# Optimization experiments

Measured on AMD Instinct MI355X. Metric: run time of the kernel, lower is better.

## Reference

```python
import jax, jax.numpy as jnp
import numpy as np


def setup_inputs() -> dict:
    key = jax.random.key(0)
    k1, k2, k3, k4 = jax.random.split(key, 4)
    batch, d_in, d_out, K, M = 4096, 1024, 1024, 16, 512
    x = jax.random.normal(k1, (batch, d_in), dtype=jnp.float32)
    A = jax.random.normal(k2, (K, d_in, M), dtype=jnp.float32) * (1.0 / np.sqrt(d_in))
    B = jax.random.normal(k3, (K, M, d_out), dtype=jnp.float32) * (1.0 / np.sqrt(M))
    bias = jnp.zeros((d_out,), dtype=jnp.float32)
    topk_mask = jax.random.randint(k4, (batch, K), 0, 2) > 0
    return {"x": x, "topk_mask": topk_mask, "A": A, "B": B, "bias": bias}


def reference(x, topk_mask, A, B, bias):
    # pre_inner_acts: [batch, k, m]
    pre = jnp.einsum('bi,kim->bkm', x, A)
    maskf = topk_mask.astype(pre.dtype)[:, :, None]  # [batch, k, 1]
    pre = pre * maskf
    # inner_acts: [batch, k, out]
    inner_acts = jnp.einsum('bkm,kmh->bkh', pre, B)
    inner_acts = inner_acts * maskf
    out = jnp.sum(inner_acts, axis=1) + bias  # [batch, out]
    return out, inner_acts
```

## Files before the change

kernel.cpp:

```cpp
#include <hip/hip_runtime.h>

typedef __attribute__((ext_vector_type(8))) short bf16x8;
typedef __attribute__((ext_vector_type(4))) float f32x4;

__device__ __forceinline__ unsigned short f2bf(float f) {
  union { float f; unsigned u; } v; v.f = f;
  unsigned r = v.u + 0x7fffu + ((v.u >> 16) & 1u);
  return (unsigned short)(r >> 16);
}

__global__ __launch_bounds__(256)
void prep_kernel(const float* __restrict__ x, unsigned short* __restrict__ x_bf,
                 const float* __restrict__ A, unsigned short* __restrict__ A_t,
                 const float* __restrict__ B, unsigned short* __restrict__ B_t,
                 const int* __restrict__ mask, int* __restrict__ rows,
                 int* __restrict__ counts) {
  __shared__ float tbuf[32][33];
  __shared__ int cnt, mcnt;
  const int bid = blockIdx.x;
  const int t = threadIdx.x;

  if (bid < 4096) {
    int i = bid * 256 + t;
    float4 v = ((const float4*)x)[i];
    ushort4 o; o.x = f2bf(v.x); o.y = f2bf(v.y); o.z = f2bf(v.z); o.w = f2bf(v.w);
    ((ushort4*)x_bf)[i] = o;
    return;
  }
  if (bid < 20480) {
    const float* in; unsigned short* out; int R, C, cx, ry, z;
    if (bid < 12288) {
      int local = (bid - 4096) & 511; z = (bid - 4096) >> 9;
      R = 1024; C = 512; cx = local & 15; ry = local >> 4;
      in = A; out = A_t;
    } else {
      int local = (bid - 12288) & 511; z = (bid - 12288) >> 9;
      R = 512; C = 1024; cx = local & 31; ry = local >> 5;
      in = B; out = B_t;
    }
    size_t eo = (size_t)z * R * C;
    const float* src = in + eo;
    unsigned short* dst = out + eo;
    int c0 = cx * 32, r0 = ry * 32;
    int tx = t & 31, ty = t >> 5;
#pragma unroll
    for (int i = 0; i < 32; i += 8)
      tbuf[ty + i][tx] = src[(size_t)(r0 + ty + i) * C + (c0 + tx)];
    __syncthreads();
#pragma unroll
    for (int i = 0; i < 32; i += 8)
      dst[(size_t)(c0 + ty + i) * R + (r0 + tx)] = f2bf(tbuf[tx][ty + i]);
    return;
  }
  {
    int z = bid - 20480;
    if (t == 0) { cnt = 0; mcnt = 0; }
    __syncthreads();
    int* rz = rows + (size_t)z * 4096;
    for (int i = t; i < 4096; i += 256) {
      bool m = mask[(size_t)i * 16 + z] != 0;
      unsigned long long bal = __ballot(m);
      int lane = t & 63;
      int pa = __popcll(bal & ((1ull << lane) - 1ull));
      int ta = __popcll(bal);
      int base_a, base_m;
      if (lane == 0) { base_a = atomicAdd(&cnt, ta); base_m = atomicAdd(&mcnt, 64 - ta); }
      base_a = __shfl(base_a, 0);
      base_m = __shfl(base_m, 0);
      int pm = lane - pa;
      if (m) rz[base_a + pa] = i;
      else   rz[4095 - (base_m + pm)] = i;
    }
    __syncthreads();
    if (t == 0) counts[z] = cnt;
  }
}

__device__ __forceinline__ void stage_tile(const unsigned short* __restrict__ src,
                                           size_t row_stride, int row0, int k0,
                                           unsigned short* lds) {
  int t = threadIdx.x;
  int lane = t & 63;
  int w = t >> 6;
#pragma unroll
  for (int i = 0; i < 4; ++i) {
    int chunk = w * 4 + i;
    int row = chunk * 8 + (lane >> 3);
    int glog = (lane & 7) ^ (row & 7);
    const unsigned short* g = src + (size_t)(row0 + row) * row_stride + (size_t)(k0 + glog * 8);
    __builtin_amdgcn_global_load_lds((const __attribute__((address_space(1))) unsigned int*)g,
                                     (__attribute__((address_space(3))) unsigned int*)(lds + chunk * 512),
                                     16, 0, 0);
  }
}

__device__ __forceinline__ void stage_tile_gather(const unsigned short* __restrict__ src,
                                                  const int* __restrict__ rowsS, int k0,
                                                  unsigned short* lds) {
  int t = threadIdx.x;
  int lane = t & 63;
  int w = t >> 6;
#pragma unroll
  for (int i = 0; i < 4; ++i) {
    int chunk = w * 4 + i;
    int row = chunk * 8 + (lane >> 3);
    int glog = (lane & 7) ^ (row & 7);
    const unsigned short* g = src + (size_t)rowsS[row] * 1024 + (size_t)(k0 + glog * 8);
    __builtin_amdgcn_global_load_lds((const __attribute__((address_space(1))) unsigned int*)g,
                                     (__attribute__((address_space(3))) unsigned int*)(lds + chunk * 512),
                                     16, 0, 0);
  }
}

__device__ __forceinline__ bf16x8 read_frag(const unsigned short* lds, int row, int gb) {
  int phys = (row * 128 + gb) ^ ((row & 7) << 4);
  return *(const bf16x8*)((const char*)lds + phys);
}

template <int MODE>
__global__ __launch_bounds__(256)
void moe_gemm_kernel(const unsigned short* __restrict__ X,
                     const unsigned short* __restrict__ W,
                     unsigned short* __restrict__ pre_out,
                     float* __restrict__ inner_out,
                     const int* __restrict__ rows,
                     const int* __restrict__ counts) {
  const int gx = gridDim.x, gy = gridDim.y;
  {
    int lin = blockIdx.x + gx * (blockIdx.y + gy * blockIdx.z);
    int cpx = (gx * gy * gridDim.z) >> 3;
    lin = (lin & 7) * cpx + (lin >> 3);
    int bx = lin % gx; lin /= gx;
    int by = lin % gy; lin /= gy;
    const int z = lin;
    const int cnt = counts[z];
    const int tb = by * 128;
    const int tn = bx * 128;
    const int t = threadIdx.x;

    if (MODE == 0 && tb >= cnt) return;

    __shared__ unsigned short Xs[128 * 64];
    __shared__ unsigned short Ws[128 * 64];
    __shared__ int rowsS[128];

    if (t < 128) rowsS[t] = rows[(size_t)z * 4096 + tb + t];
    __syncthreads();

    if (MODE == 1 && tb >= cnt) {
      const float4 z4 = {0.f, 0.f, 0.f, 0.f};
#pragma unroll
      for (int it = 0; it < 16; ++it) {
        int rl = it * 8 + (t >> 5);
        int b = rowsS[rl];
        ((float4*)(inner_out + (size_t)b * (16 * 1024) + (size_t)z * 1024 + tn))[t & 31] = z4;
      }
      return;
    }

    const int lane = t & 63;
    const int wv = t >> 6;
    const int wr = (wv >> 1) * 64;
    const int wc = (wv & 1) * 64;
    const int fr = lane & 15;
    const int fg = lane >> 4;

    const unsigned short* Xbase;
    const unsigned short* Wbase;
    size_t xstride, wstride;
    int nkt;
    if (MODE == 0) {
      Xbase = X;                            xstride = 1024;
      Wbase = W + (size_t)z * 512 * 1024;   wstride = 1024;
      nkt = 16;
    } else {
      Xbase = X + (size_t)z * 4096 * 512;   xstride = 512;
      Wbase = W + (size_t)z * 1024 * 512;   wstride = 512;
      nkt = 8;
    }

    f32x4 acc[4][4] = {};

    for (int kt = 0; kt < nkt; ++kt) {
      if (kt) __syncthreads();
      if (MODE == 0) stage_tile_gather(Xbase, rowsS, kt * 64, Xs);
      else           stage_tile(Xbase, xstride, tb, kt * 64, Xs);
      stage_tile(Wbase, wstride, tn, kt * 64, Ws);
      __syncthreads();
#pragma unroll
      for (int kk = 0; kk < 2; ++kk) {
        const int gb = kk * 64 + fg * 16;
        bf16x8 xf[4], wf[4];
#pragma unroll
        for (int i = 0; i < 4; ++i) {
          xf[i] = read_frag(Xs, wr + i * 16 + fr, gb);
          wf[i] = read_frag(Ws, wc + i * 16 + fr, gb);
        }
#pragma unroll
        for (int mi = 0; mi < 4; ++mi)
#pragma unroll
          for (int ni = 0; ni < 4; ++ni)
            acc[mi][ni] = __builtin_amdgcn_mfma_f32_16x16x32_bf16(xf[mi], wf[ni], acc[mi][ni], 0, 0, 0);
      }
    }

    if (MODE == 0) {
#pragma unroll
      for (int mi = 0; mi < 4; ++mi) {
#pragma unroll
        for (int j = 0; j < 4; ++j) {
          int rl = wr + mi * 16 + fg * 4 + j;
          size_t rowbase = (size_t)z * 4096 * 512 + (size_t)(tb + rl) * 512;
#pragma unroll
          for (int ni = 0; ni < 4; ++ni) {
            int m = tn + wc + ni * 16 + fr;
            pre_out[rowbase + m] = f2bf(acc[mi][ni][j]);
          }
        }
      }
    } else {
#pragma unroll
      for (int mi = 0; mi < 4; ++mi) {
#pragma unroll
        for (int j = 0; j < 4; ++j) {
          int rl = wr + mi * 16 + fg * 4 + j;
          int b = rowsS[rl];
          size_t rowbase = (size_t)b * (16 * 1024) + (size_t)z * 1024;
          if (tb + rl < cnt) {
#pragma unroll
            for (int ni = 0; ni < 4; ++ni) {
              int h = tn + wc + ni * 16 + fr;
              inner_out[rowbase + h] = acc[mi][ni][j];
            }
          } else {
#pragma unroll
            for (int ni = 0; ni < 4; ++ni) {
              int h = tn + wc + ni * 16 + fr;
              inner_out[rowbase + h] = 0.f;
            }
          }
        }
      }
    }
  }
}

__global__ __launch_bounds__(256)
void reduce_kernel(const float* __restrict__ inner, const float* __restrict__ bias,
                   const int* __restrict__ mask, float* __restrict__ out) {
  int b = blockIdx.x;
  int t = threadIdx.x;
  __shared__ int mrow[16];
  if (t < 16) mrow[t] = mask[(size_t)b * 16 + t];
  __syncthreads();
  float4 s = ((const float4*)bias)[t];
  const float4* ip = (const float4*)(inner + (size_t)b * (16 * 1024)) + t;
#pragma unroll
  for (int k = 0; k < 16; ++k) {
    if (mrow[k]) {
      float4 v = ip[(size_t)k * 256];
      s.x += v.x; s.y += v.y; s.z += v.z; s.w += v.w;
    }
  }
  ((float4*)out)[(size_t)b * 256 + t] = s;
}

extern "C" void kernel_launch(void* const* d_in, const int* in_sizes, int n_in,
                              void* d_out, int out_size, void* d_ws, size_t ws_size,
                              hipStream_t stream) {
  const float* x    = (const float*)d_in[0];
  const int*   mask = (const int*)d_in[1];
  const float* A    = (const float*)d_in[2];
  const float* B    = (const float*)d_in[3];
  const float* bias = (const float*)d_in[4];

  float* out   = (float*)d_out;
  float* inner = (float*)d_out + (size_t)4096 * 1024;

  if (ws_size < 109314112ull) return;
  char* ws = (char*)d_ws;
  unsigned short* x_bf = (unsigned short*)ws;
  unsigned short* A_t  = (unsigned short*)(ws + ((size_t)8 << 20));
  unsigned short* B_t  = (unsigned short*)(ws + ((size_t)24 << 20));
  unsigned short* pre  = (unsigned short*)(ws + ((size_t)40 << 20));
  int* rows            = (int*)(ws + ((size_t)104 << 20));
  int* counts          = (int*)(ws + ((size_t)104 << 20) + 262144);

  prep_kernel<<<20496, 256, 0, stream>>>(x, x_bf, A, A_t, B, B_t, mask, rows, counts);

  moe_gemm_kernel<0><<<dim3(4, 32, 16), 256, 0, stream>>>(x_bf, A_t, pre, nullptr, rows, counts);
  moe_gemm_kernel<1><<<dim3(8, 32, 16), 256, 0, stream>>>(pre, B_t, nullptr, inner, rows, counts);

  reduce_kernel<<<4096, 256, 0, stream>>>(inner, bias, mask, out);
}
```

Measured before the change: 189.6 us.

## Overlap B weight transpose with first GEMM inside one fused launch

The B transpose/bf16 conversion moves out of the prep kernel and into the first GEMM launch as extra blocks, so the transpose traffic can run concurrently with GEMM1 tiles instead of serially before them. Block indices are remapped so each XCD-like chunk gets both GEMM and transpose work. GEMM1 now allocates the transpose scratch in shared memory too, which may lower occupancy, and the empty GEMM tiles exit early.

Result: slower. 194.1 us (+2.4%).

```diff
diff --git a/kernel.cpp b/kernel.cpp
--- a/kernel.cpp
+++ b/kernel.cpp
@@ -12,7 +12,6 @@
 __global__ __launch_bounds__(256)
 void prep_kernel(const float* __restrict__ x, unsigned short* __restrict__ x_bf,
                  const float* __restrict__ A, unsigned short* __restrict__ A_t,
-                 const float* __restrict__ B, unsigned short* __restrict__ B_t,
                  const int* __restrict__ mask, int* __restrict__ rows,
                  int* __restrict__ counts) {
   __shared__ float tbuf[32][33];
@@ -27,20 +26,14 @@
     ((ushort4*)x_bf)[i] = o;
     return;
   }
-  if (bid < 20480) {
-    const float* in; unsigned short* out; int R, C, cx, ry, z;
-    if (bid < 12288) {
-      int local = (bid - 4096) & 511; z = (bid - 4096) >> 9;
-      R = 1024; C = 512; cx = local & 15; ry = local >> 4;
-      in = A; out = A_t;
-    } else {
-      int local = (bid - 12288) & 511; z = (bid - 12288) >> 9;
-      R = 512; C = 1024; cx = local & 31; ry = local >> 5;
-      in = B; out = B_t;
-    }
+  if (bid < 12288) {
+    int local = (bid - 4096) & 511;
+    int z = (bid - 4096) >> 9;
+    const int R = 1024, C = 512;
+    int cx = local & 15, ry = local >> 4;
     size_t eo = (size_t)z * R * C;
-    const float* src = in + eo;
-    unsigned short* dst = out + eo;
+    const float* src = A + eo;
+    unsigned short* dst = A_t + eo;
     int c0 = cx * 32, r0 = ry * 32;
     int tx = t & 31, ty = t >> 5;
 #pragma unroll
@@ -53,7 +46,7 @@
     return;
   }
   {
-    int z = bid - 20480;
+    int z = bid - 12288;
     if (t == 0) { cnt = 0; mcnt = 0; }
     __syncthreads();
     int* rz = rows + (size_t)z * 4096;
@@ -117,128 +110,193 @@
   return *(const bf16x8*)((const char*)lds + phys);
 }
 
-template <int MODE>
 __global__ __launch_bounds__(256)
-void moe_gemm_kernel(const unsigned short* __restrict__ X,
-                     const unsigned short* __restrict__ W,
-                     unsigned short* __restrict__ pre_out,
-                     float* __restrict__ inner_out,
-                     const int* __restrict__ rows,
-                     const int* __restrict__ counts) {
+void gemm1_fused_kernel(const unsigned short* __restrict__ X,
+                        const unsigned short* __restrict__ W,
+                        unsigned short* __restrict__ pre_out,
+                        const float* __restrict__ B, unsigned short* __restrict__ B_t,
+                        const int* __restrict__ rows,
+                        const int* __restrict__ counts) {
+  __shared__ unsigned short Xs[128 * 64];
+  __shared__ unsigned short Ws[128 * 64];
+  __shared__ int rowsS[128];
+  __shared__ float tbuf[32][33];
+
+  const int o = blockIdx.x;
+  const int chunk = o & 7;
+  const int pos = o >> 3;
+  const int t = threadIdx.x;
+
+  if (pos >= 256) {
+    int tr = chunk * 1024 + (pos - 256);
+    int z = tr >> 9;
+    int local = tr & 511;
+    const int R = 512, C = 1024;
+    int cx = local & 31, ry = local >> 5;
+    size_t eo = (size_t)z * R * C;
+    const float* src = B + eo;
+    unsigned short* dst = B_t + eo;
+    int c0 = cx * 32, r0 = ry * 32;
+    int tx = t & 31, ty = t >> 5;
+#pragma unroll
+    for (int i = 0; i < 32; i += 8)
+      tbuf[ty + i][tx] = src[(size_t)(r0 + ty + i) * C + (c0 + tx)];
+    __syncthreads();
+#pragma unroll
+    for (int i = 0; i < 32; i += 8)
+      dst[(size_t)(c0 + ty + i) * R + (r0 + tx)] = f2bf(tbuf[tx][ty + i]);
+    return;
+  }
+
+  int g = chunk * 256 + pos;
+  const int bx = g & 3;
+  const int by = (g >> 2) & 31;
+  const int z = g >> 7;
+
+  const int cnt = counts[z];
+  const int tb = by * 128;
+  const int tn = bx * 128;
+  if (tb >= cnt) return;
+
+  if (t < 128) rowsS[t] = rows[(size_t)z * 4096 + tb + t];
+  __syncthreads();
+
+  const int lane = t & 63;
+  const int wv = t >> 6;
+  const int wr = (wv >> 1) * 64;
+  const int wc = (wv & 1) * 64;
+  const int fr = lane & 15;
+  const int fg = lane >> 4;
+
+  const unsigned short* Wbase = W + (size_t)z * 512 * 1024;
+
+  f32x4 acc[4][4] = {};
+
+  for (int kt = 0; kt < 16; ++kt) {
+    if (kt) __syncthreads();
+    stage_tile_gather(X, rowsS, kt * 64, Xs);
+    stage_tile(Wbase, 1024, tn, kt * 64, Ws);
+    __syncthreads();
+#pragma unroll
+    for (int kk = 0; kk < 2; ++kk) {
+      const int gb = kk * 64 + fg * 16;
+      bf16x8 xf[4], wf[4];
+#pragma unroll
+      for (int i = 0; i < 4; ++i) {
+        xf[i] = read_frag(Xs, wr + i * 16 + fr, gb);
+        wf[i] = read_frag(Ws, wc + i * 16 + fr, gb);
+      }
+#pragma unroll
+      for (int mi = 0; mi < 4; ++mi)
+#pragma unroll
+        for (int ni = 0; ni < 4; ++ni)
+          acc[mi][ni] = __builtin_amdgcn_mfma_f32_16x16x32_bf16(xf[mi], wf[ni], acc[mi][ni], 0, 0, 0);
+    }
+  }
+
+#pragma unroll
+  for (int mi = 0; mi < 4; ++mi) {
+#pragma unroll
+    for (int j = 0; j < 4; ++j) {
+      int rl = wr + mi * 16 + fg * 4 + j;
+      size_t rowbase = (size_t)z * 4096 * 512 + (size_t)(tb + rl) * 512;
+#pragma unroll
+      for (int ni = 0; ni < 4; ++ni) {
+        int m = tn + wc + ni * 16 + fr;
+        pre_out[rowbase + m] = f2bf(acc[mi][ni][j]);
+      }
+    }
+  }
+}
+
+__global__ __launch_bounds__(256)
+void gemm2_kernel(const unsigned short* __restrict__ X,
+                  const unsigned short* __restrict__ W,
+                  float* __restrict__ inner_out,
+                  const int* __restrict__ rows,
+                  const int* __restrict__ counts) {
   const int gx = gridDim.x, gy = gridDim.y;
-  {
-    int lin = blockIdx.x + gx * (blockIdx.y + gy * blockIdx.z);
-    int cpx = (gx * gy * gridDim.z) >> 3;
-    lin = (lin & 7) * cpx + (lin >> 3);
-    int bx = lin % gx; lin /= gx;
-    int by = lin % gy; lin /= gy;
-    const int z = lin;
-    const int cnt = counts[z];
-    const int tb = by * 128;
-    const int tn = bx * 128;
-    const int t = threadIdx.x;
-
-    if (MODE == 0 && tb >= cnt) return;
-
-    __shared__ unsigned short Xs[128 * 64];
-    __shared__ unsigned short Ws[128 * 64];
-    __shared__ int rowsS[128];
-
-    if (t < 128) rowsS[t] = rows[(size_t)z * 4096 + tb + t];
-    __syncthreads();
-
-    if (MODE == 1 && tb >= cnt) {
-      const float4 z4 = {0.f, 0.f, 0.f, 0.f};
-#pragma unroll
-      for (int it = 0; it < 16; ++it) {
-        int rl = it * 8 + (t >> 5);
-        int b = rowsS[rl];
-        ((float4*)(inner_out + (size_t)b * (16 * 1024) + (size_t)z * 1024 + tn))[t & 31] = z4;
+  int lin = blockIdx.x + gx * (blockIdx.y + gy * blockIdx.z);
+  int cpx = (gx * gy * gridDim.z) >> 3;
+  lin = (lin & 7) * cpx + (lin >> 3);
+  int bx = lin % gx; lin /= gx;
+  int by = lin % gy; lin /= gy;
+  const int z = lin;
+  const int cnt = counts[z];
+  const int tb = by * 128;
+  const int tn = bx * 128;
+  const int t = threadIdx.x;
+
+  __shared__ unsigned short Xs[128 * 64];
+  __shared__ unsigned short Ws[128 * 64];
+  __shared__ int rowsS[128];
+
+  if (t < 128) rowsS[t] = rows[(size_t)z * 4096 + tb + t];
+  __syncthreads();
+
+  if (tb >= cnt) {
+    const float4 z4 = {0.f, 0.f, 0.f, 0.f};
+#pragma unroll
+    for (int it = 0; it < 16; ++it) {
+      int rl = it * 8 + (t >> 5);
+      int b = rowsS[rl];
+      ((float4*)(inner_out + (size_t)b * (16 * 1024) + (size_t)z * 1024 + tn))[t & 31] = z4;
+    }
+    return;
+  }
+
+  const int lane = t & 63;
+  const int wv = t >> 6;
+  const int wr = (wv >> 1) * 64;
+  const int wc = (wv & 1) * 64;
+  const int fr = lane & 15;
+  const int fg = lane >> 4;
+
+  const unsigned short* Xbase = X + (size_t)z * 4096 * 512;
+  const unsigned short* Wbase = W + (size_t)z * 1024 * 512;
+
+  f32x4 acc[4][4] = {};
+
+  for (int kt = 0; kt < 8; ++kt) {
+    if (kt) __syncthreads();
+    stage_tile(Xbase, 512, tb, kt * 64, Xs);
+    stage_tile(Wbase, 512, tn, kt * 64, Ws);
+    __syncthreads();
+#pragma unroll
+    for (int kk = 0; kk < 2; ++kk) {
+      const int gb = kk * 64 + fg * 16;
+      bf16x8 xf[4], wf[4];
+#pragma unroll
+      for (int i = 0; i < 4; ++i) {
+        xf[i] = read_frag(Xs, wr + i * 16 + fr, gb);
+        wf[i] = read_frag(Ws, wc + i * 16 + fr, gb);
       }
-      return;
-    }
-
-    const int lane = t & 63;
-    const int wv = t >> 6;
-    const int wr = (wv >> 1) * 64;
-    const int wc = (wv & 1) * 64;
-    const int fr = lane & 15;
-    const int fg = lane >> 4;
-
-    const unsigned short* Xbase;
-    const unsigned short* Wbase;
-    size_t xstride, wstride;
-    int nkt;
-    if (MODE == 0) {
-      Xbase = X;                            xstride = 1024;
-      Wbase = W + (size_t)z * 512 * 1024;   wstride = 1024;
-      nkt = 16;
-    } else {
-      Xbase = X + (size_t)z * 4096 * 512;   xstride = 512;
-      Wbase = W + (size_t)z * 1024 * 512;   wstride = 512;
-      nkt = 8;
-    }
-
-    f32x4 acc[4][4] = {};
-
-    for (int kt = 0; kt < nkt; ++kt) {
-      if (kt) __syncthreads();
-      if (MODE == 0) stage_tile_gather(Xbase, rowsS, kt * 64, Xs);
-      else           stage_tile(Xbase, xstride, tb, kt * 64, Xs);
-      stage_tile(Wbase, wstride, tn, kt * 64, Ws);
-      __syncthreads();
-#pragma unroll
-      for (int kk = 0; kk < 2; ++kk) {
-        const int gb = kk * 64 + fg * 16;
-        bf16x8 xf[4], wf[4];
-#pragma unroll
-        for (int i = 0; i < 4; ++i) {
-          xf[i] = read_frag(Xs, wr + i * 16 + fr, gb);
-          wf[i] = read_frag(Ws, wc + i * 16 + fr, gb);
+#pragma unroll
+      for (int mi = 0; mi < 4; ++mi)
+#pragma unroll
+        for (int ni = 0; ni < 4; ++ni)
+          acc[mi][ni] = __builtin_amdgcn_mfma_f32_16x16x32_bf16(xf[mi], wf[ni], acc[mi][ni], 0, 0, 0);
+    }
+  }
+
+#pragma unroll
+  for (int mi = 0; mi < 4; ++mi) {
+#pragma unroll
+    for (int j = 0; j < 4; ++j) {
+      int rl = wr + mi * 16 + fg * 4 + j;
+      int b = rowsS[rl];
+      size_t rowbase = (size_t)b * (16 * 1024) + (size_t)z * 1024;
+      if (tb + rl < cnt) {
+#pragma unroll
+        for (int ni = 0; ni < 4; ++ni) {
+          int h = tn + wc + ni * 16 + fr;
+          inner_out[rowbase + h] = acc[mi][ni][j];
         }
-#pragma unroll
-        for (int mi = 0; mi < 4; ++mi)
-#pragma unroll
-          for (int ni = 0; ni < 4; ++ni)
-            acc[mi][ni] = __builtin_amdgcn_mfma_f32_16x16x32_bf16(xf[mi], wf[ni], acc[mi][ni], 0, 0, 0);
-      }
-    }
-
-    if (MODE == 0) {
-#pragma unroll
-      for (int mi = 0; mi < 4; ++mi) {
-#pragma unroll
-        for (int j = 0; j < 4; ++j) {
-          int rl = wr + mi * 16 + fg * 4 + j;
-          size_t rowbase = (size_t)z * 4096 * 512 + (size_t)(tb + rl) * 512;
-#pragma unroll
-          for (int ni = 0; ni < 4; ++ni) {
-            int m = tn + wc + ni * 16 + fr;
-            pre_out[rowbase + m] = f2bf(acc[mi][ni][j]);
-          }
-        }
-      }
-    } else {
-#pragma unroll
-      for (int mi = 0; mi < 4; ++mi) {
-#pragma unroll
-        for (int j = 0; j < 4; ++j) {
-          int rl = wr + mi * 16 + fg * 4 + j;
-          int b = rowsS[rl];
-          size_t rowbase = (size_t)b * (16 * 1024) + (size_t)z * 1024;
-          if (tb + rl < cnt) {
-#pragma unroll
-            for (int ni = 0; ni < 4; ++ni) {
-              int h = tn + wc + ni * 16 + fr;
-              inner_out[rowbase + h] = acc[mi][ni][j];
-            }
-          } else {
-#pragma unroll
-            for (int ni = 0; ni < 4; ++ni) {
-              int h = tn + wc + ni * 16 + fr;
-              inner_out[rowbase + h] = 0.f;
-            }
-          }
+      } else {
+#pragma unroll
+        for (int ni = 0; ni < 4; ++ni) {
+          int h = tn + wc + ni * 16 + fr;
+          inner_out[rowbase + h] = 0.f;
         }
       }
     }
@@ -286,10 +344,10 @@
   int* rows            = (int*)(ws + ((size_t)104 << 20));
   int* counts          = (int*)(ws + ((size_t)104 << 20) + 262144);
 
-  prep_kernel<<<20496, 256, 0, stream>>>(x, x_bf, A, A_t, B, B_t, mask, rows, counts);
-
-  moe_gemm_kernel<0><<<dim3(4, 32, 16), 256, 0, stream>>>(x_bf, A_t, pre, nullptr, rows, counts);
-  moe_gemm_kernel<1><<<dim3(8, 32, 16), 256, 0, stream>>>(pre, B_t, nullptr, inner, rows, counts);
+  prep_kernel<<<12304, 256, 0, stream>>>(x, x_bf, A, A_t, mask, rows, counts);
+
+  gemm1_fused_kernel<<<10240, 256, 0, stream>>>(x_bf, A_t, pre, B, B_t, rows, counts);
+  gemm2_kernel<<<dim3(8, 32, 16), 256, 0, stream>>>(pre, B_t, inner, rows, counts);
 
   reduce_kernel<<<4096, 256, 0, stream>>>(inner, bias, mask, out);
 }
```
